# Performance work log

Hardware: AMD Instinct MI355X
Metric: run time of the kernel (lower is better)

The kernel has to match this reference:

```python
import jax, jax.numpy as jnp
import numpy as np

B, T, H, V, C = 8192, 40, 128, 4450, 102

def setup_inputs() -> dict:
    key = jax.random.key(0)
    ks = jax.random.split(key, 9)
    s = 1.0 / np.sqrt(H)
    return {
        "input_ids": jax.random.randint(ks[0], (B, T), 0, V, dtype=jnp.int64),
        "emb_c": jax.random.normal(ks[1], (V, H), jnp.float32),
        "emb_a": jax.random.normal(ks[2], (V, H), jnp.float32),
        "W_ih": jax.random.uniform(ks[3], (3 * H, H), jnp.float32, -s, s),
        "W_hh": jax.random.uniform(ks[4], (3 * H, H), jnp.float32, -s, s),
        "b_ih": jax.random.uniform(ks[5], (3 * H,), jnp.float32, -s, s),
        "b_hh": jax.random.uniform(ks[6], (3 * H,), jnp.float32, -s, s),
        "W_cls": jax.random.uniform(ks[7], (C, H), jnp.float32, -s, s),
        "b_cls": jax.random.uniform(ks[8], (C,), jnp.float32, -s, s),
    }

def _gru_scan(x_seq, W_ih, W_hh, b_ih, b_hh):
    # x_seq: [T, B, H]; PyTorch GRU gate order: r, z, n
    h0 = jnp.zeros((x_seq.shape[1], H), x_seq.dtype)
    def step(h, x):
        gi = x @ W_ih.T + b_ih          # [B, 3H]
        gh = h @ W_hh.T + b_hh          # [B, 3H]
        i_r, i_z, i_n = jnp.split(gi, 3, axis=-1)
        h_r, h_z, h_n = jnp.split(gh, 3, axis=-1)
        r = jax.nn.sigmoid(i_r + h_r)
        z = jax.nn.sigmoid(i_z + h_z)
        n = jnp.tanh(i_n + r * h_n)
        h_new = (1.0 - z) * n + z * h
        return h_new, h_new
    _, hs = jax.lax.scan(step, h0, x_seq)
    return hs                            # [T, B, H]

def reference(input_ids, emb_c, emb_a, W_ih, W_hh, b_ih, b_hh, W_cls, b_cls):
    x_a = emb_a[input_ids].transpose(1, 0, 2)   # [T, B, H]
    x_c = emb_c[input_ids].transpose(1, 0, 2)
    ha = _gru_scan(x_a, W_ih, W_hh, b_ih, b_hh).transpose(1, 0, 2)  # [B, T, H]
    hc = _gru_scan(x_c, W_ih, W_hh, b_ih, b_hh).transpose(1, 0, 2)
    matrix = jnp.einsum('bth,bsh->bts', ha, ha)  # [B, T, T]
    A = jax.nn.softmax(matrix, axis=1)           # Softmax(dim=1) over 3D
    attn = A.transpose(0, 2, 1)                  # [B, T, T]
    # bmm(hc^T [B,H,T], attn).transpose -> out[b,s,h] = sum_t hc[b,t,h]*attn[b,t,s]
    out = jnp.einsum('bth,bts->bsh', hc, attn)   # [B, T, H]
    logits = out.reshape(-1, H) @ W_cls.T + b_cls  # [B*T, C]
    return jax.nn.softmax(logits, axis=1)
```

## Files before the change

kernel.cpp:

```cpp
#include <hip/hip_runtime.h>
#include <hip/hip_bf16.h>

#define BB 8192
#define TT 40
#define HH 128
#define CC 102
#define VV 4450

typedef __attribute__((ext_vector_type(8))) short short8;
typedef __attribute__((ext_vector_type(4))) float f4;

__device__ __forceinline__ float rcpf_(float x) { return __builtin_amdgcn_rcpf(x); }
__device__ __forceinline__ float sigmoidf_(float x) { return rcpf_(1.f + __expf(-x)); }
__device__ __forceinline__ float tanhf_(float x) { float e = __expf(2.f * x); return 1.f - 2.f * rcpf_(e + 1.f); }

__device__ __forceinline__ unsigned short f2bf(float x) {
    union { float f; unsigned u; } v; v.f = x;
    unsigned r = v.u + 0x7FFFu + ((v.u >> 16) & 1u);
    return (unsigned short)(r >> 16);
}
__device__ __forceinline__ float bf2f(unsigned short h) {
    union { float f; unsigned u; } v; v.u = ((unsigned)h) << 16; return v.f;
}
__device__ __forceinline__ short8 u4s8(uint4 v) { return *(short8*)&v; }

__device__ __forceinline__ unsigned cvtpk_bf16(float lo, float hi) {
    unsigned r;
    asm("v_cvt_pk_bf16_f32 %0, %1, %2" : "=v"(r) : "v"(lo), "v"(hi));
    return r;
}
__device__ __forceinline__ void split2(float a, float b, unsigned& H, unsigned& L) {
    H = cvtpk_bf16(a, b);
    float ra = __uint_as_float(H << 16);
    float rb = __uint_as_float(H & 0xFFFF0000u);
    L = cvtpk_bf16(a - ra, b - rb);
}

struct __attribute__((aligned(4))) G3 { float r, z, n; };

#define MFMA16(acc, a, b) acc = __builtin_amdgcn_mfma_f32_16x16x32_bf16(a, b, acc, 0, 0, 0)

__global__ __launch_bounds__(256) void prep_bf16split(const float* __restrict__ W,
                                                      unsigned short* __restrict__ hi,
                                                      unsigned short* __restrict__ lo, int n) {
    int i = blockIdx.x * 256 + threadIdx.x;
    if (i < n) {
        float x = W[i];
        unsigned short h = f2bf(x);
        hi[i] = h;
        lo[i] = f2bf(x - bf2f(h));
    }
}

__global__ __launch_bounds__(256) void prep_wcls(const float* __restrict__ W,
                                                 unsigned short* __restrict__ hi,
                                                 unsigned short* __restrict__ lo) {
    int i = blockIdx.x * 256 + threadIdx.x;
    if (i < 112 * HH) {
        int r = i >> 7;
        float x = (r < CC) ? W[i] : 0.f;
        unsigned short h = f2bf(x);
        hi[i] = h;
        lo[i] = f2bf(x - bf2f(h));
    }
}

__global__ __launch_bounds__(256) void prep_G_mfma(
    const float* __restrict__ emb_a, const float* __restrict__ emb_c,
    const unsigned short* __restrict__ WihH, const unsigned short* __restrict__ WihL,
    const float* __restrict__ b_ih, const float* __restrict__ b_hh,
    float* __restrict__ G)
{
    __shared__ uint4 se[2][32][16];

    const int tid = threadIdx.x;
    const int src = blockIdx.y;
    const float* emb = src ? emb_c : emb_a;
    const int v0 = blockIdx.x * 32;

    const int lane = tid & 63;
    const int w = tid >> 6;
    const int mcol = lane & 15;
    const int quad = lane >> 4;

#pragma unroll
    for (int i = 0; i < 4; ++i) {
        int task = tid + 256 * i;
        int row = task >> 5, q = task & 31;
        int v = v0 + row;
        float4 x = make_float4(0.f, 0.f, 0.f, 0.f);
        if (v < VV) x = ((const float4*)(emb + (size_t)v * HH))[q];
        uint2 Hw, Lw;
        split2(x.x, x.y, Hw.x, Lw.x);
        split2(x.z, x.w, Hw.y, Lw.y);
        int phys = (q >> 1) ^ (row & 15);
        ((uint2*)&se[0][row][phys])[q & 1] = Hw;
        ((uint2*)&se[1][row][phys])[q & 1] = Lw;
    }

    float bias[6];
#pragma unroll
    for (int n6 = 0; n6 < 6; ++n6) {
        int c = w * 96 + n6 * 16 + mcol;
        bias[n6] = b_ih[c] + (c < 256 ? b_hh[c] : 0.f);
    }

    f4 acc[2][6];
#pragma unroll
    for (int mt = 0; mt < 2; ++mt)
#pragma unroll
        for (int n6 = 0; n6 < 6; ++n6) acc[mt][n6] = (f4){0.f, 0.f, 0.f, 0.f};

    __syncthreads();

#pragma unroll
    for (int kk = 0; kk < 4; ++kk) {
        uint4 bH[6], bL[6];
#pragma unroll
        for (int n6 = 0; n6 < 6; ++n6) {
            int rowc = w * 96 + n6 * 16 + mcol;
            bH[n6] = *((const uint4*)WihH + rowc * 16 + kk * 4 + quad);
            bL[n6] = *((const uint4*)WihL + rowc * 16 + kk * 4 + quad);
        }
#pragma unroll
        for (int mt = 0; mt < 2; ++mt) {
            int m = mt * 16 + mcol;
            int phys = (kk * 4 + quad) ^ mcol;
            short8 ah = u4s8(se[0][m][phys]);
            short8 al = u4s8(se[1][m][phys]);
#pragma unroll
            for (int n6 = 0; n6 < 6; ++n6) {
                MFMA16(acc[mt][n6], ah, u4s8(bH[n6]));
                MFMA16(acc[mt][n6], ah, u4s8(bL[n6]));
                MFMA16(acc[mt][n6], al, u4s8(bH[n6]));
            }
        }
    }

    float* gout = G + (size_t)src * VV * 384;
#pragma unroll
    for (int mt = 0; mt < 2; ++mt)
#pragma unroll
        for (int r = 0; r < 4; ++r) {
            int m = mt * 16 + quad * 4 + r;
            int v = v0 + m;
            if (v < VV) {
#pragma unroll
                for (int n6 = 0; n6 < 6; ++n6) {
                    int c = w * 96 + n6 * 16 + mcol;
                    int g = c >> 7, j = c & 127;
                    gout[(size_t)v * 384 + j * 3 + g] = acc[mt][n6][r] + bias[n6];
                }
            }
        }
}

__global__ __launch_bounds__(512, 2) void gru_mfma(
    const int* __restrict__ ids, const float* __restrict__ G,
    const __hip_bfloat16* __restrict__ Whi, const __hip_bfloat16* __restrict__ Wlo,
    const float* __restrict__ b_hh, float* __restrict__ ha, float* __restrict__ hc)
{
    __shared__ uint4 sh[2][2][32][16];
    __shared__ int sids[32 * TT];

    const int tid = threadIdx.x;
    const int src = blockIdx.y;
    const int b0 = blockIdx.x * 32;
    const float* Gs = G + (size_t)src * VV * 384;
    float* hout = src ? hc : ha;

    const int lane = tid & 63;
    const int w = tid >> 6;
    const int nc0 = w * 16;
    const int mcol = lane & 15;
    const int quad = lane >> 4;

    for (int idx = tid; idx < 32 * TT; idx += 512)
        sids[idx] = ids[b0 * TT + idx];

    {
        uint4 z; z.x = z.y = z.z = z.w = 0u;
        uint4* p = &sh[0][0][0][0];
        for (int idx = tid; idx < 2 * 32 * 16; idx += 512) p[idx] = z;
    }

    short8 bh[3][4], bl[3][4];
#pragma unroll
    for (int g = 0; g < 3; ++g)
#pragma unroll
        for (int kk = 0; kk < 4; ++kk) {
            int row = g * 128 + nc0 + mcol;
            uint4 vh = *((const uint4*)Whi + row * 16 + kk * 4 + quad);
            uint4 vl = *((const uint4*)Wlo + row * 16 + kk * 4 + quad);
            bh[g][kk] = u4s8(vh);
            bl[g][kk] = u4s8(vl);
        }

    const int j = nc0 + mcol;
    const float bhn = b_hh[256 + j];
    const float* gbase = Gs + 3 * j;

    f4 hreg[2];
    hreg[0] = (f4){0.f, 0.f, 0.f, 0.f};
    hreg[1] = (f4){0.f, 0.f, 0.f, 0.f};

    __syncthreads();

    G3 gc[2][4];
#pragma unroll
    for (int mt = 0; mt < 2; ++mt)
#pragma unroll
        for (int reg = 0; reg < 4; ++reg) {
            int m = mt * 16 + quad * 4 + reg;
            int id = sids[m * TT + 0];
            gc[mt][reg] = *(const G3*)(gbase + (size_t)id * 384);
        }

    const int s_slot = j >> 3;
    const int jb = j & 7;

    int buf = 0;
#pragma unroll 1
    for (int t = 0; t < TT; ++t) {
        f4 acc[3][2];
#pragma unroll
        for (int g = 0; g < 3; ++g)
#pragma unroll
            for (int mt = 0; mt < 2; ++mt) acc[g][mt] = (f4){0.f, 0.f, 0.f, 0.f};

#pragma unroll
        for (int mt = 0; mt < 2; ++mt)
#pragma unroll
            for (int kk = 0; kk < 4; ++kk) {
                int m = mt * 16 + mcol;
                int phys = (kk * 4 + quad) ^ mcol;
                uint4 avh = sh[buf][0][m][phys];
                uint4 avl = sh[buf][1][m][phys];
                short8 ah = u4s8(avh), al = u4s8(avl);
#pragma unroll
                for (int g = 0; g < 3; ++g) {
                    MFMA16(acc[g][mt], ah, bh[g][kk]);
                    MFMA16(acc[g][mt], ah, bl[g][kk]);
                    MFMA16(acc[g][mt], al, bh[g][kk]);
                }
            }

        const int nbuf = buf ^ 1;
#pragma unroll
        for (int mt = 0; mt < 2; ++mt) {
            float hv4[4];
#pragma unroll
            for (int reg = 0; reg < 4; ++reg) {
                G3 g = gc[mt][reg];
                float rr = sigmoidf_(acc[0][mt][reg] + g.r);
                float zz = sigmoidf_(acc[1][mt][reg] + g.z);
                float nn = tanhf_(g.n + rr * (acc[2][mt][reg] + bhn));
                float hv = fmaf(zz, hreg[mt][reg] - nn, nn);
                hreg[mt][reg] = hv;
                hv4[reg] = hv;

                int m = mt * 16 + quad * 4 + reg;
                hout[((size_t)(b0 + m) * TT + t) * HH + j] = hv;
            }
#pragma unroll
            for (int pr = 0; pr < 2; ++pr) {
                unsigned Hp, Lp;
                split2(hv4[pr * 2], hv4[pr * 2 + 1], Hp, Lp);
#pragma unroll
                for (int k = 0; k < 2; ++k) {
                    int m = mt * 16 + quad * 4 + pr * 2 + k;
                    int phys = s_slot ^ (m & 15);
                    unsigned short hb = (unsigned short)(k ? (Hp >> 16) : Hp);
                    unsigned short lb = (unsigned short)(k ? (Lp >> 16) : Lp);
                    ((unsigned short*)&sh[nbuf][0][m][phys])[jb] = hb;
                    ((unsigned short*)&sh[nbuf][1][m][phys])[jb] = lb;
                }
            }
        }

        if (t < TT - 1) {
#pragma unroll
            for (int mt = 0; mt < 2; ++mt)
#pragma unroll
                for (int reg = 0; reg < 4; ++reg) {
                    int m = mt * 16 + quad * 4 + reg;
                    int id = sids[m * TT + t + 1];
                    gc[mt][reg] = *(const G3*)(gbase + (size_t)id * 384);
                }
        }
        __syncthreads();
        buf ^= 1;
    }
}

#define AT_SHA     0
#define AT_SHA_LO  12288
#define AT_SHCT    24576
#define AT_SHCT_LO 40960
#define AT_SM      57344
#define AT_SW      66752
#define AT_SW_LO   72896
#define AT_PARTM   79040
#define AT_PARTD   79808
#define AT_SMX     80576
#define AT_SDI     80768
#define AT_TOTAL   80960

__global__ __launch_bounds__(256, 2) void attn_cls_mfma(
    const float* __restrict__ ha, const float* __restrict__ hc,
    const unsigned short* __restrict__ WcH, const unsigned short* __restrict__ WcL,
    const float* __restrict__ b_cls, float* __restrict__ out)
{
    __shared__ __attribute__((aligned(16))) char smem[AT_TOTAL];
    const int tid = threadIdx.x;
    const int lane = tid & 63;
    const int w = tid >> 6;
    const int quad = lane >> 4;
    const int col = lane & 15;
    const size_t b = blockIdx.x;

    float* sm    = (float*)(smem + AT_SM);
    float* slog  = (float*)(smem + AT_SM);
    float* partM = (float*)(smem + AT_PARTM);
    float* partD = (float*)(smem + AT_PARTD);
    float* sMX   = (float*)(smem + AT_SMX);
    float* sDI   = (float*)(smem + AT_SDI);

    const int ntc0 = (w < 3) ? w : 3;
    const int ntc1 = (w < 3) ? w + 4 : 3;
    uint4 bw[2][4][2];
    float bcv[2];
    {
        int nts[2] = {ntc0, ntc1};
#pragma unroll
        for (int which = 0; which < 2; ++which) {
            int row = nts[which] * 16 + col;
#pragma unroll
            for (int kk = 0; kk < 4; ++kk) {
                bw[which][kk][0] = *((const uint4*)WcH + row * 16 + kk * 4 + quad);
                bw[which][kk][1] = *((const uint4*)WcL + row * 16 + kk * 4 + quad);
            }
            bcv[which] = (row < CC) ? b_cls[row] : 0.f;
        }
    }

    {
        const float4* hab = (const float4*)(ha + b * TT * HH);
#pragma unroll
        for (int i = 0; i < 5; ++i) {
            int f4i = tid + 256 * i;
            int row = f4i >> 5, q = f4i & 31;
            float4 v = hab[f4i];
            uint2 Hw, Lw;
            split2(v.x, v.y, Hw.x, Lw.x);
            split2(v.z, v.w, Hw.y, Lw.y);
            int phys = (q >> 1) ^ (row & 15);
            int off = row * 256 + phys * 16 + (q & 1) * 8;
            *(uint2*)(smem + AT_SHA + off) = Hw;
            *(uint2*)(smem + AT_SHA_LO + off) = Lw;
        }
        if (tid < 128) {
            int row = 40 + (tid >> 4), c = tid & 15;
            uint4 z; z.x = z.y = z.z = z.w = 0u;
            *(uint4*)(smem + AT_SHA + row * 256 + c * 16) = z;
            *(uint4*)(smem + AT_SHA_LO + row * 256 + c * 16) = z;
        }
        const float* hcb = hc + b * TT * HH;
        for (int task = tid; task < 640; task += 256) {
            int h = task & 127, c = task >> 7;
            float x[8];
#pragma unroll
            for (int jj = 0; jj < 8; ++jj) x[jj] = hcb[(c * 8 + jj) * HH + h];
            uint4 Hq, Lq;
            split2(x[0], x[1], Hq.x, Lq.x);
            split2(x[2], x[3], Hq.y, Lq.y);
            split2(x[4], x[5], Hq.z, Lq.z);
            split2(x[6], x[7], Hq.w, Lq.w);
            int phys = c ^ (h & 7);
            *(uint4*)(smem + AT_SHCT + h * 128 + phys * 16) = Hq;
            *(uint4*)(smem + AT_SHCT_LO + h * 128 + phys * 16) = Lq;
        }
        for (int task = tid; task < 384; task += 256) {
            int h = task & 127, c = 5 + (task >> 7);
            int phys = c ^ (h & 7);
            uint4 z; z.x = z.y = z.z = z.w = 0u;
            *(uint4*)(smem + AT_SHCT + h * 128 + phys * 16) = z;
            *(uint4*)(smem + AT_SHCT_LO + h * 128 + phys * 16) = z;
        }
    }
    __syncthreads();

    if (w < 3) {
        const int mt = w;
        uint4 aH[4], aL[4];
#pragma unroll
        for (int kk = 0; kk < 4; ++kk) {
            int phys = (kk * 4 + quad) ^ col;
            int off = (mt * 16 + col) * 256 + phys * 16;
            aH[kk] = *(uint4*)(smem + AT_SHA + off);
            aL[kk] = *(uint4*)(smem + AT_SHA_LO + off);
        }
        f4 acc[3];
#pragma unroll
        for (int nt = 0; nt < 3; ++nt) acc[nt] = (f4){0.f, 0.f, 0.f, 0.f};
#pragma unroll
        for (int kk = 0; kk < 4; ++kk) {
            short8 ah = u4s8(aH[kk]), al = u4s8(aL[kk]);
#pragma unroll
            for (int nt = 0; nt < 3; ++nt) {
                int phys = (kk * 4 + quad) ^ col;
                int off = (nt * 16 + col) * 256 + phys * 16;
                short8 bH = u4s8(*(uint4*)(smem + AT_SHA + off));
                short8 bL = u4s8(*(uint4*)(smem + AT_SHA_LO + off));
                MFMA16(acc[nt], ah, bH);
                MFMA16(acc[nt], ah, bL);
                MFMA16(acc[nt], al, bH);
            }
        }
#pragma unroll
        for (int nt = 0; nt < 3; ++nt)
#pragma unroll
            for (int r = 0; r < 4; ++r)
                sm[(mt * 16 + quad * 4 + r) * 49 + nt * 16 + col] = acc[nt][r];
    }
    __syncthreads();

    if (tid < 160) {
        int t = tid >> 2, p = tid & 3;
        const float* row = sm + t * 49 + p * 10;
        float M = row[0];
#pragma unroll
        for (int i = 1; i < 10; ++i) M = fmaxf(M, row[i]);
        float D = 0.f;
#pragma unroll
        for (int i = 0; i < 10; ++i) D += __expf(row[i] - M);
        partM[t * 4 + p] = M;
        partD[t * 4 + p] = D;
    }
    __syncthreads();
    if (tid < 40) {
        float M = partM[tid * 4];
        M = fmaxf(M, partM[tid * 4 + 1]); M = fmaxf(M, partM[tid * 4 + 2]); M = fmaxf(M, partM[tid * 4 + 3]);
        float D = 0.f;
#pragma unroll
        for (int p = 0; p < 4; ++p) D += partD[tid * 4 + p] * __expf(partM[tid * 4 + p] - M);
        sMX[tid] = M;
        sDI[tid] = rcpf_(D);
    }
    __syncthreads();

    for (int task = tid; task < 384; task += 256) {
        int s = task >> 3, c = task & 7;
        uint4 Hq, Lq;
        if (c >= 5) {
            Hq.x = Hq.y = Hq.z = Hq.w = 0u; Lq = Hq;
        } else {
            const float* srow = sm + s * 49 + c * 8;
            float wv[8];
#pragma unroll
            for (int jj = 0; jj < 8; ++jj) {
                int t = c * 8 + jj;
                wv[jj] = __expf(srow[jj] - sMX[t]) * sDI[t];
            }
            split2(wv[0], wv[1], Hq.x, Lq.x);
            split2(wv[2], wv[3], Hq.y, Lq.y);
            split2(wv[4], wv[5], Hq.z, Lq.z);
            split2(wv[6], wv[7], Hq.w, Lq.w);
        }
        int phys = c ^ (s & 7);
        *(uint4*)(smem + AT_SW + s * 128 + phys * 16) = Hq;
        *(uint4*)(smem + AT_SW_LO + s * 128 + phys * 16) = Lq;
    }
    __syncthreads();

    {
        uint4 aH[3][2], aL[3][2];
#pragma unroll
        for (int mt = 0; mt < 3; ++mt)
#pragma unroll
            for (int kk = 0; kk < 2; ++kk) {
                int s = mt * 16 + col;
                int phys = (kk * 4 + quad) ^ (s & 7);
                aH[mt][kk] = *(uint4*)(smem + AT_SW + s * 128 + phys * 16);
                aL[mt][kk] = *(uint4*)(smem + AT_SW_LO + s * 128 + phys * 16);
            }
        f4 acc[3][2];
#pragma unroll
        for (int mt = 0; mt < 3; ++mt) { acc[mt][0] = (f4){0,0,0,0}; acc[mt][1] = (f4){0,0,0,0}; }
#pragma unroll
        for (int which = 0; which < 2; ++which) {
            int nt = w + which * 4;
            int hrow = nt * 16 + col;
#pragma unroll
            for (int kk = 0; kk < 2; ++kk) {
                int phys = (kk * 4 + quad) ^ (hrow & 7);
                short8 bH = u4s8(*(uint4*)(smem + AT_SHCT + hrow * 128 + phys * 16));
                short8 bL = u4s8(*(uint4*)(smem + AT_SHCT_LO + hrow * 128 + phys * 16));
#pragma unroll
                for (int mt = 0; mt < 3; ++mt) {
                    short8 ah = u4s8(aH[mt][kk]), al = u4s8(aL[mt][kk]);
                    MFMA16(acc[mt][which], ah, bH);
                    MFMA16(acc[mt][which], ah, bL);
                    MFMA16(acc[mt][which], al, bH);
                }
            }
        }
        __syncthreads();
#pragma unroll
        for (int which = 0; which < 2; ++which) {
            int h = (w + which * 4) * 16 + col;
            int chunk = h >> 3, hb7 = (h & 7) * 2;
#pragma unroll
            for (int mt = 0; mt < 3; ++mt)
#pragma unroll
                for (int pr = 0; pr < 2; ++pr) {
                    unsigned Hp, Lp;
                    split2(acc[mt][which][pr * 2], acc[mt][which][pr * 2 + 1], Hp, Lp);
#pragma unroll
                    for (int k = 0; k < 2; ++k) {
                        int s = mt * 16 + quad * 4 + pr * 2 + k;
                        int phys = chunk ^ (s & 15);
                        *(unsigned short*)(smem + AT_SHA + s * 256 + phys * 16 + hb7) =
                            (unsigned short)(k ? (Hp >> 16) : Hp);
                        *(unsigned short*)(smem + AT_SHA_LO + s * 256 + phys * 16 + hb7) =
                            (unsigned short)(k ? (Lp >> 16) : Lp);
                    }
                }
        }
    }
    __syncthreads();

    {
        f4 acc[3][2];
#pragma unroll
        for (int mt = 0; mt < 3; ++mt) { acc[mt][0] = (f4){0,0,0,0}; acc[mt][1] = (f4){0,0,0,0}; }
#pragma unroll
        for (int kk = 0; kk < 4; ++kk)
#pragma unroll
            for (int mt = 0; mt < 3; ++mt) {
                int s = mt * 16 + col;
                int phys = (kk * 4 + quad) ^ (s & 15);
                short8 ah = u4s8(*(uint4*)(smem + AT_SHA + s * 256 + phys * 16));
                short8 al = u4s8(*(uint4*)(smem + AT_SHA_LO + s * 256 + phys * 16));
#pragma unroll
                for (int which = 0; which < 2; ++which) {
                    MFMA16(acc[mt][which], ah, u4s8(bw[which][kk][0]));
                    MFMA16(acc[mt][which], ah, u4s8(bw[which][kk][1]));
                    MFMA16(acc[mt][which], al, u4s8(bw[which][kk][0]));
                }
            }
        __syncthreads();
        int nts[2] = {ntc0, ntc1};
#pragma unroll
        for (int which = 0; which < 2; ++which) {
            int c = nts[which] * 16 + col;
#pragma unroll
            for (int mt = 0; mt < 3; ++mt)
#pragma unroll
                for (int r = 0; r < 4; ++r)
                    slog[(mt * 16 + quad * 4 + r) * 113 + c] = acc[mt][which][r] + bcv[which];
        }
    }
    __syncthreads();

    if (tid < 160) {
        int s = tid >> 2, p = tid & 3;
        int c0 = p * 26;
        int c1 = (c0 + 26 < CC) ? c0 + 26 : CC;
        const float* row = slog + s * 113;
        float M = row[c0];
        for (int c = c0 + 1; c < c1; ++c) M = fmaxf(M, row[c]);
        float D = 0.f;
        for (int c = c0; c < c1; ++c) D += __expf(row[c] - M);
        partM[s * 4 + p] = M;
        partD[s * 4 + p] = D;
    }
    __syncthreads();
    if (tid < 40) {
        float M = partM[tid * 4];
        M = fmaxf(M, partM[tid * 4 + 1]); M = fmaxf(M, partM[tid * 4 + 2]); M = fmaxf(M, partM[tid * 4 + 3]);
        float D = 0.f;
#pragma unroll
        for (int p = 0; p < 4; ++p) D += partD[tid * 4 + p] * __expf(partM[tid * 4 + p] - M);
        sMX[tid] = M;
        sDI[tid] = rcpf_(D);
    }
    __syncthreads();

    {
        int c = tid & 127, s0 = tid >> 7;
        if (c < CC) {
            float* ob = out + b * TT * CC;
            for (int s = s0; s < TT; s += 2)
                ob[s * CC + c] = __expf(slog[s * 113 + c] - sMX[s]) * sDI[s];
        }
    }
}

extern "C" void kernel_launch(void* const* d_in, const int* in_sizes, int n_in,
                              void* d_out, int out_size, void* d_ws, size_t ws_size,
                              hipStream_t stream) {
    const int*   ids   = (const int*)d_in[0];
    const float* emb_c = (const float*)d_in[1];
    const float* emb_a = (const float*)d_in[2];
    const float* W_ih  = (const float*)d_in[3];
    const float* W_hh  = (const float*)d_in[4];
    const float* b_ih  = (const float*)d_in[5];
    const float* b_hh  = (const float*)d_in[6];
    const float* W_cls = (const float*)d_in[7];
    const float* b_cls = (const float*)d_in[8];
    float* out = (float*)d_out;

    float* ha = (float*)d_ws;
    float* hc = ha + (size_t)BB * TT * HH;
    float* G  = hc + (size_t)BB * TT * HH;
    __hip_bfloat16* Whi = (__hip_bfloat16*)(G + (size_t)2 * VV * 384);
    __hip_bfloat16* Wlo = Whi + 384 * HH;
    unsigned short* WcH = (unsigned short*)(Wlo + 384 * HH);
    unsigned short* WcL = WcH + 112 * HH;
    unsigned short* WihH = WcL + 112 * HH;
    unsigned short* WihL = WihH + 384 * HH;

    prep_bf16split<<<(384 * HH + 255) / 256, 256, 0, stream>>>(W_hh, (unsigned short*)Whi, (unsigned short*)Wlo, 384 * HH);
    prep_bf16split<<<(384 * HH + 255) / 256, 256, 0, stream>>>(W_ih, WihH, WihL, 384 * HH);
    prep_wcls<<<(112 * HH + 255) / 256, 256, 0, stream>>>(W_cls, WcH, WcL);
    prep_G_mfma<<<dim3((VV + 31) / 32, 2), 256, 0, stream>>>(emb_a, emb_c, WihH, WihL, b_ih, b_hh, G);
    gru_mfma<<<dim3(BB / 32, 2), 512, 0, stream>>>(ids, G, Whi, Wlo, b_hh, ha, hc);
    attn_cls_mfma<<<BB, 256, 0, stream>>>(ha, hc, WcH, WcL, b_cls, out);
}
```

Before: 603.6 us.

## Fuse both GRU sequences into one block and use exp2 with prescaled weights

```diff
diff --git a/kernel.cpp b/kernel.cpp
--- a/kernel.cpp
+++ b/kernel.cpp
@@ -7,12 +7,14 @@
 #define CC 102
 #define VV 4450
 
+#define L2E  1.4426950408889634f
+#define L2E2 2.8853900817779268f
+
 typedef __attribute__((ext_vector_type(8))) short short8;
 typedef __attribute__((ext_vector_type(4))) float f4;
 
 __device__ __forceinline__ float rcpf_(float x) { return __builtin_amdgcn_rcpf(x); }
-__device__ __forceinline__ float sigmoidf_(float x) { return rcpf_(1.f + __expf(-x)); }
-__device__ __forceinline__ float tanhf_(float x) { float e = __expf(2.f * x); return 1.f - 2.f * rcpf_(e + 1.f); }
+__device__ __forceinline__ float exp2f_(float x) { return __builtin_amdgcn_exp2f(x); }
 
 __device__ __forceinline__ unsigned short f2bf(float x) {
     union { float f; unsigned u; } v; v.f = x;
@@ -46,6 +48,19 @@
     int i = blockIdx.x * 256 + threadIdx.x;
     if (i < n) {
         float x = W[i];
+        unsigned short h = f2bf(x);
+        hi[i] = h;
+        lo[i] = f2bf(x - bf2f(h));
+    }
+}
+
+__global__ __launch_bounds__(256) void prep_whh(const float* __restrict__ W,
+                                                unsigned short* __restrict__ hi,
+                                                unsigned short* __restrict__ lo) {
+    int i = blockIdx.x * 256 + threadIdx.x;
+    if (i < 384 * HH) {
+        float s = (i < 256 * HH) ? L2E : L2E2;
+        float x = W[i] * s;
         unsigned short h = f2bf(x);
         hi[i] = h;
         lo[i] = f2bf(x - bf2f(h));
@@ -148,26 +163,24 @@
 #pragma unroll
                 for (int n6 = 0; n6 < 6; ++n6) {
                     int c = w * 96 + n6 * 16 + mcol;
-                    int g = c >> 7, j = c & 127;
-                    gout[(size_t)v * 384 + j * 3 + g] = acc[mt][n6][r] + bias[n6];
+                    int g = c >> 7, jj = c & 127;
+                    float scl = (g < 2) ? L2E : L2E2;
+                    gout[(size_t)v * 384 + jj * 3 + g] = (acc[mt][n6][r] + bias[n6]) * scl;
                 }
             }
         }
 }
 
-__global__ __launch_bounds__(512, 2) void gru_mfma(
+__global__ __launch_bounds__(512, 1) void gru_mfma(
     const int* __restrict__ ids, const float* __restrict__ G,
     const __hip_bfloat16* __restrict__ Whi, const __hip_bfloat16* __restrict__ Wlo,
     const float* __restrict__ b_hh, float* __restrict__ ha, float* __restrict__ hc)
 {
-    __shared__ uint4 sh[2][2][32][16];
+    __shared__ uint4 sh[2][2][2][32][16];
     __shared__ int sids[32 * TT];
 
     const int tid = threadIdx.x;
-    const int src = blockIdx.y;
     const int b0 = blockIdx.x * 32;
-    const float* Gs = G + (size_t)src * VV * 384;
-    float* hout = src ? hc : ha;
 
     const int lane = tid & 63;
     const int w = tid >> 6;
@@ -180,8 +193,10 @@
 
     {
         uint4 z; z.x = z.y = z.z = z.w = 0u;
-        uint4* p = &sh[0][0][0][0];
-        for (int idx = tid; idx < 2 * 32 * 16; idx += 512) p[idx] = z;
+        for (int idx = tid; idx < 1024; idx += 512) {
+            (&sh[0][0][0][0][0])[idx] = z;
+            (&sh[1][0][0][0][0])[idx] = z;
+        }
     }
 
     short8 bh[3][4], bl[3][4];
@@ -197,96 +212,93 @@
         }
 
     const int j = nc0 + mcol;
-    const float bhn = b_hh[256 + j];
-    const float* gbase = Gs + 3 * j;
-
-    f4 hreg[2];
-    hreg[0] = (f4){0.f, 0.f, 0.f, 0.f};
-    hreg[1] = (f4){0.f, 0.f, 0.f, 0.f};
-
-    __syncthreads();
-
-    G3 gc[2][4];
-#pragma unroll
-    for (int mt = 0; mt < 2; ++mt)
-#pragma unroll
-        for (int reg = 0; reg < 4; ++reg) {
-            int m = mt * 16 + quad * 4 + reg;
-            int id = sids[m * TT + 0];
-            gc[mt][reg] = *(const G3*)(gbase + (size_t)id * 384);
-        }
+    const float bhn = L2E2 * b_hh[256 + j];
+    const float* gb0 = G + 3 * j;
+    const float* gb1 = G + (size_t)VV * 384 + 3 * j;
+
+    f4 hreg[2][2];
+    hreg[0][0] = (f4){0.f,0.f,0.f,0.f}; hreg[0][1] = (f4){0.f,0.f,0.f,0.f};
+    hreg[1][0] = (f4){0.f,0.f,0.f,0.f}; hreg[1][1] = (f4){0.f,0.f,0.f,0.f};
 
     const int s_slot = j >> 3;
     const int jb = j & 7;
+
+    __syncthreads();
 
     int buf = 0;
 #pragma unroll 1
     for (int t = 0; t < TT; ++t) {
-        f4 acc[3][2];
-#pragma unroll
-        for (int g = 0; g < 3; ++g)
-#pragma unroll
-            for (int mt = 0; mt < 2; ++mt) acc[g][mt] = (f4){0.f, 0.f, 0.f, 0.f};
-
+        G3 gc[2][2][4];
 #pragma unroll
         for (int mt = 0; mt < 2; ++mt)
 #pragma unroll
-            for (int kk = 0; kk < 4; ++kk) {
-                int m = mt * 16 + mcol;
-                int phys = (kk * 4 + quad) ^ mcol;
-                uint4 avh = sh[buf][0][m][phys];
-                uint4 avl = sh[buf][1][m][phys];
-                short8 ah = u4s8(avh), al = u4s8(avl);
-#pragma unroll
-                for (int g = 0; g < 3; ++g) {
-                    MFMA16(acc[g][mt], ah, bh[g][kk]);
-                    MFMA16(acc[g][mt], ah, bl[g][kk]);
-                    MFMA16(acc[g][mt], al, bh[g][kk]);
+            for (int reg = 0; reg < 4; ++reg) {
+                int m = mt * 16 + quad * 4 + reg;
+                int id = sids[m * TT + t];
+                gc[0][mt][reg] = *(const G3*)(gb0 + (size_t)id * 384);
+                gc[1][mt][reg] = *(const G3*)(gb1 + (size_t)id * 384);
+            }
+
+        f4 acc[2][3][2];
+#pragma unroll
+        for (int s = 0; s < 2; ++s)
+#pragma unroll
+            for (int g = 0; g < 3; ++g)
+#pragma unroll
+                for (int mt = 0; mt < 2; ++mt) acc[s][g][mt] = (f4){0.f, 0.f, 0.f, 0.f};
+
+#pragma unroll
+        for (int s = 0; s < 2; ++s)
+#pragma unroll
+            for (int mt = 0; mt < 2; ++mt)
+#pragma unroll
+                for (int kk = 0; kk < 4; ++kk) {
+                    int m = mt * 16 + mcol;
+                    int phys = (kk * 4 + quad) ^ mcol;
+                    short8 ah = u4s8(sh[s][buf][0][m][phys]);
+                    short8 al = u4s8(sh[s][buf][1][m][phys]);
+#pragma unroll
+                    for (int g = 0; g < 3; ++g) {
+                        MFMA16(acc[s][g][mt], ah, bh[g][kk]);
+                        MFMA16(acc[s][g][mt], ah, bl[g][kk]);
+                        MFMA16(acc[s][g][mt], al, bh[g][kk]);
+                    }
                 }
-            }
 
         const int nbuf = buf ^ 1;
 #pragma unroll
-        for (int mt = 0; mt < 2; ++mt) {
-            float hv4[4];
-#pragma unroll
-            for (int reg = 0; reg < 4; ++reg) {
-                G3 g = gc[mt][reg];
-                float rr = sigmoidf_(acc[0][mt][reg] + g.r);
-                float zz = sigmoidf_(acc[1][mt][reg] + g.z);
-                float nn = tanhf_(g.n + rr * (acc[2][mt][reg] + bhn));
-                float hv = fmaf(zz, hreg[mt][reg] - nn, nn);
-                hreg[mt][reg] = hv;
-                hv4[reg] = hv;
-
-                int m = mt * 16 + quad * 4 + reg;
-                hout[((size_t)(b0 + m) * TT + t) * HH + j] = hv;
-            }
-#pragma unroll
-            for (int pr = 0; pr < 2; ++pr) {
-                unsigned Hp, Lp;
-                split2(hv4[pr * 2], hv4[pr * 2 + 1], Hp, Lp);
-#pragma unroll
-                for (int k = 0; k < 2; ++k) {
-                    int m = mt * 16 + quad * 4 + pr * 2 + k;
-                    int phys = s_slot ^ (m & 15);
-                    unsigned short hb = (unsigned short)(k ? (Hp >> 16) : Hp);
-                    unsigned short lb = (unsigned short)(k ? (Lp >> 16) : Lp);
-                    ((unsigned short*)&sh[nbuf][0][m][phys])[jb] = hb;
-                    ((unsigned short*)&sh[nbuf][1][m][phys])[jb] = lb;
+        for (int s = 0; s < 2; ++s) {
+            float* houts = s ? hc : ha;
+#pragma unroll
+            for (int mt = 0; mt < 2; ++mt) {
+#pragma unroll
+                for (int reg = 0; reg < 4; ++reg) {
+                    G3 g = gc[s][mt][reg];
+                    float rr = rcpf_(1.f + exp2f_(-(acc[s][0][mt][reg] + g.r)));
+                    float zz = rcpf_(1.f + exp2f_(-(acc[s][1][mt][reg] + g.z)));
+                    float y  = g.n + rr * (acc[s][2][mt][reg] + bhn);
+                    float nn = 1.f - 2.f * rcpf_(exp2f_(y) + 1.f);
+                    float hv = fmaf(zz, hreg[s][mt][reg] - nn, nn);
+                    hreg[s][mt][reg] = hv;
+
+                    int m = mt * 16 + quad * 4 + reg;
+                    houts[((size_t)(b0 + m) * TT + t) * HH + j] = hv;
                 }
-            }
-        }
-
-        if (t < TT - 1) {
-#pragma unroll
-            for (int mt = 0; mt < 2; ++mt)
-#pragma unroll
-                for (int reg = 0; reg < 4; ++reg) {
-                    int m = mt * 16 + quad * 4 + reg;
-                    int id = sids[m * TT + t + 1];
-                    gc[mt][reg] = *(const G3*)(gbase + (size_t)id * 384);
+#pragma unroll
+                for (int pr = 0; pr < 2; ++pr) {
+                    unsigned Hp, Lp;
+                    split2(hreg[s][mt][pr * 2], hreg[s][mt][pr * 2 + 1], Hp, Lp);
+#pragma unroll
+                    for (int k = 0; k < 2; ++k) {
+                        int m = mt * 16 + quad * 4 + pr * 2 + k;
+                        int phys = s_slot ^ (m & 15);
+                        ((unsigned short*)&sh[s][nbuf][0][m][phys])[jb] =
+                            (unsigned short)(k ? (Hp >> 16) : Hp);
+                        ((unsigned short*)&sh[s][nbuf][1][m][phys])[jb] =
+                            (unsigned short)(k ? (Lp >> 16) : Lp);
+                    }
                 }
+            }
         }
         __syncthreads();
         buf ^= 1;
@@ -621,10 +633,10 @@
     unsigned short* WihH = WcL + 112 * HH;
     unsigned short* WihL = WihH + 384 * HH;
 
-    prep_bf16split<<<(384 * HH + 255) / 256, 256, 0, stream>>>(W_hh, (unsigned short*)Whi, (unsigned short*)Wlo, 384 * HH);
+    prep_whh<<<(384 * HH + 255) / 256, 256, 0, stream>>>(W_hh, (unsigned short*)Whi, (unsigned short*)Wlo);
     prep_bf16split<<<(384 * HH + 255) / 256, 256, 0, stream>>>(W_ih, WihH, WihL, 384 * HH);
     prep_wcls<<<(112 * HH + 255) / 256, 256, 0, stream>>>(W_cls, WcH, WcL);
     prep_G_mfma<<<dim3((VV + 31) / 32, 2), 256, 0, stream>>>(emb_a, emb_c, WihH, WihL, b_ih, b_hh, G);
-    gru_mfma<<<dim3(BB / 32, 2), 512, 0, stream>>>(ids, G, Whi, Wlo, b_hh, ha, hc);
+    gru_mfma<<<dim3(BB / 32), 512, 0, stream>>>(ids, G, Whi, Wlo, b_hh, ha, hc);
     attn_cls_mfma<<<BB, 256, 0, stream>>>(ha, hc, WcH, WcL, b_cls, out);
 }
```

Result: slower. 690.0 us (+14.3%).
